# Performance work log

Hardware: AMD Instinct MI355X
Metric: run time of the kernel (lower is better)

The kernel has to match this reference:

```python
import jax, jax.numpy as jnp
import numpy as np

EMBED = 1024
NUM_HEADS = 8
HEAD_DIM = EMBED // NUM_HEADS // 2  # 64
LAMBDA_INIT = 0.8
EPS = 1e-5


def setup_inputs() -> dict:
    key = jax.random.key(0)
    ks = jax.random.split(key, 12)
    B, T = 2, 2048
    mk = lambda k, shape, s=1.0: (jax.random.normal(k, shape, dtype=jnp.float32) * s)
    return {
        "q": mk(ks[0], (B, T, EMBED)),
        "k": mk(ks[1], (B, T, EMBED)),
        "v": mk(ks[2], (B, T, EMBED)),
        "Wq": mk(ks[3], (EMBED, EMBED), EMBED ** -0.5),
        "Wk": mk(ks[4], (EMBED, EMBED), EMBED ** -0.5),
        "Wv": mk(ks[5], (EMBED, EMBED), EMBED ** -0.5),
        "Wo": mk(ks[6], (EMBED, EMBED), EMBED ** -0.5),
        "lambda_q1": mk(ks[7], (HEAD_DIM,), 0.1),
        "lambda_k1": mk(ks[8], (HEAD_DIM,), 0.1),
        "lambda_q2": mk(ks[9], (HEAD_DIM,), 0.1),
        "lambda_k2": mk(ks[10], (HEAD_DIM,), 0.1),
    }


def reference(q, k, v, Wq, Wk, Wv, Wo, lambda_q1, lambda_k1, lambda_q2, lambda_k2):
    B, T, E = q.shape
    H, d = NUM_HEADS, HEAD_DIM
    scaling = d ** -0.5
    # projections (torch Linear: x @ W^T)
    qh = (q @ Wq.T).reshape(B, T, 2 * H, d).transpose(0, 2, 1, 3) * scaling  # [B,2H,T,d]
    kh = (k @ Wk.T).reshape(B, T, 2 * H, d).transpose(0, 2, 1, 3)            # [B,2H,T,d]
    vh = (v @ Wv.T).reshape(B, T, H, 2 * d).transpose(0, 2, 1, 3)            # [B,H,T,2d]
    # dual softmax attention over doubled heads
    attn_weights = jnp.einsum("bhtd,bhsd->bhts", qh, kh)  # [B,2H,T,S]
    attn_weights = jax.nn.softmax(attn_weights, axis=-1)
    # lambda-weighted difference
    lambda_1 = jnp.exp(jnp.sum(lambda_q1 * lambda_k1))
    lambda_2 = jnp.exp(jnp.sum(lambda_q2 * lambda_k2))
    lambda_full = lambda_1 - lambda_2 + LAMBDA_INIT
    aw = attn_weights.reshape(B, H, 2, T, T)
    aw = aw[:, :, 0] - lambda_full * aw[:, :, 1]  # [B,H,T,S]
    attn = jnp.einsum("bhts,bhsd->bhtd", aw, vh)  # [B,H,T,2d]
    # RMSNorm over last dim (no affine), then rescale
    attn = attn * jax.lax.rsqrt(jnp.mean(attn * attn, axis=-1, keepdims=True) + EPS)
    attn = attn * (1.0 - LAMBDA_INIT)
    attn = attn.transpose(0, 2, 1, 3).reshape(B, T, H * 2 * d)
    return attn @ Wo.T
```

## Files before the change

kernel.cpp:

```cpp
#include <hip/hip_runtime.h>
#include <hip/hip_bf16.h>

typedef __bf16 bf16;
typedef __attribute__((ext_vector_type(8))) __bf16 bf16x8;
typedef __attribute__((ext_vector_type(4))) __bf16 bf16x4;
typedef __attribute__((ext_vector_type(4))) float f32x4;
typedef __attribute__((ext_vector_type(16))) float f32x16;

#define EMBED 1024
#define BB 2
#define TT 2048
#define NH 8
#define MROWS (BB * TT)

__device__ __forceinline__ void async_cp16(const void* g, void* s) {
    __builtin_amdgcn_global_load_lds((const __attribute__((address_space(1))) void*)g,
                                     (__attribute__((address_space(3))) void*)s, 16, 0, 0);
}

struct Cvt7 { const float* s[7]; bf16* d[7]; int n[7]; };

__global__ __launch_bounds__(256) void cvt_kernel(Cvt7 a) {
    const int sl = blockIdx.y;
    const float* __restrict__ s = a.s[sl];
    bf16* __restrict__ d = a.d[sl];
    int i = (blockIdx.x * 256 + threadIdx.x) * 8;
    if (i >= a.n[sl]) return;
    f32x4 x = *(const f32x4*)(s + i);
    f32x4 y = *(const f32x4*)(s + i + 4);
    bf16x8 o;
    o[0] = (bf16)x[0]; o[1] = (bf16)x[1]; o[2] = (bf16)x[2]; o[3] = (bf16)x[3];
    o[4] = (bf16)y[0]; o[5] = (bf16)y[1]; o[6] = (bf16)y[2]; o[7] = (bf16)y[3];
    *(bf16x8*)(d + i) = o;
}

struct ProjArgs { const bf16* A[3]; const bf16* Bw[3]; bf16* C[3]; float scale[3]; };

__global__ __launch_bounds__(256) void gemm_proj(ProjArgs g) {
    const int z = blockIdx.z;
    const bf16* __restrict__ A  = g.A[z];
    const bf16* __restrict__ Bw = g.Bw[z];
    bf16* __restrict__ C = g.C[z];
    const float scale = g.scale[z];
    const int bm = (z == 2) ? blockIdx.y : blockIdx.x;
    const int bn = (z == 2) ? blockIdx.x : blockIdx.y;
    const int ldc = (z == 2) ? 4096 : 1024;

    __shared__ __align__(16) bf16 sA[128 * 32];
    __shared__ __align__(16) bf16 sB[128 * 32];
    const int tid = threadIdx.x;
    const int wave = tid >> 6, lane = tid & 63;
    const int wRow = (wave >> 1) * 64, wCol = (wave & 1) * 64;
    const int fr = lane & 15, fq = lane >> 4;

    f32x4 acc[4][4] = {};

    const int r = tid >> 2, jd = tid & 3;
    const int js = jd ^ ((r >> 1) & 3);
    const bf16* Ab = A + (size_t)(bm * 128 + r) * 1024 + js * 8;
    const bf16* Bb = Bw + (size_t)(bn * 128 + r) * 1024 + js * 8;

    for (int k0 = 0; k0 < 1024; k0 += 32) {
        async_cp16(Ab + k0, &sA[r * 32 + jd * 8]);
        async_cp16(Ab + (size_t)64 * 1024 + k0, &sA[(r + 64) * 32 + jd * 8]);
        async_cp16(Bb + k0, &sB[r * 32 + jd * 8]);
        async_cp16(Bb + (size_t)64 * 1024 + k0, &sB[(r + 64) * 32 + jd * 8]);
        __syncthreads();
        const int sw = (fr >> 1) & 3;
        bf16x8 af[4], bfr[4];
#pragma unroll
        for (int i = 0; i < 4; i++) {
            af[i]  = *(const bf16x8*)&sA[(wRow + 16 * i + fr) * 32 + ((fq ^ sw) * 8)];
            bfr[i] = *(const bf16x8*)&sB[(wCol + 16 * i + fr) * 32 + ((fq ^ sw) * 8)];
        }
#pragma unroll
        for (int mi = 0; mi < 4; mi++)
#pragma unroll
            for (int ni = 0; ni < 4; ni++)
                acc[mi][ni] = __builtin_amdgcn_mfma_f32_16x16x32_bf16(af[mi], bfr[ni], acc[mi][ni], 0, 0, 0);
        __syncthreads();
    }

#pragma unroll
    for (int mi = 0; mi < 4; mi++)
#pragma unroll
        for (int ni = 0; ni < 4; ni++)
#pragma unroll
            for (int rr = 0; rr < 4; rr++) {
                int row = bm * 128 + wRow + 16 * mi + fq * 4 + rr;
                int col = bn * 128 + wCol + 16 * ni + fr;
                C[(size_t)row * ldc + col] = (bf16)(acc[mi][ni][rr] * scale);
            }
}

__global__ __launch_bounds__(256) void gemm_o(const bf16* __restrict__ A,
                                              const bf16* __restrict__ Bw,
                                              float* __restrict__ C) {
    __shared__ __align__(16) bf16 sA[128 * 32];
    __shared__ __align__(16) bf16 sB[64 * 32];
    const int tid = threadIdx.x;
    const int wave = tid >> 6, lane = tid & 63;
    const int wRow = (wave >> 1) * 64, wCol = (wave & 1) * 32;
    const int bm = blockIdx.x, bn = blockIdx.y;
    const int fr = lane & 15, fq = lane >> 4;

    f32x4 acc[4][2] = {};

    const int r = tid >> 2, jd = tid & 3;
    const int js = jd ^ ((r >> 1) & 3);
    const bf16* Ab = A + (size_t)(bm * 128 + r) * 1024 + js * 8;
    const bf16* Bb = Bw + (size_t)(bn * 64 + r) * 1024 + js * 8;

    for (int k0 = 0; k0 < 1024; k0 += 32) {
        async_cp16(Ab + k0, &sA[r * 32 + jd * 8]);
        async_cp16(Ab + (size_t)64 * 1024 + k0, &sA[(r + 64) * 32 + jd * 8]);
        async_cp16(Bb + k0, &sB[r * 32 + jd * 8]);
        __syncthreads();
        const int sw = (fr >> 1) & 3;
        bf16x8 af[4], bfr[2];
#pragma unroll
        for (int i = 0; i < 4; i++)
            af[i] = *(const bf16x8*)&sA[(wRow + 16 * i + fr) * 32 + ((fq ^ sw) * 8)];
#pragma unroll
        for (int i = 0; i < 2; i++)
            bfr[i] = *(const bf16x8*)&sB[(wCol + 16 * i + fr) * 32 + ((fq ^ sw) * 8)];
#pragma unroll
        for (int mi = 0; mi < 4; mi++)
#pragma unroll
            for (int ni = 0; ni < 2; ni++)
                acc[mi][ni] = __builtin_amdgcn_mfma_f32_16x16x32_bf16(af[mi], bfr[ni], acc[mi][ni], 0, 0, 0);
        __syncthreads();
    }

#pragma unroll
    for (int mi = 0; mi < 4; mi++)
#pragma unroll
        for (int ni = 0; ni < 2; ni++)
#pragma unroll
            for (int rr = 0; rr < 4; rr++) {
                int row = bm * 128 + wRow + 16 * mi + fq * 4 + rr;
                int col = bn * 64 + wCol + 16 * ni + fr;
                C[(size_t)row * 1024 + col] = acc[mi][ni][rr];
            }
}

__global__ __launch_bounds__(512, 2) void diff_attn_mfma(const bf16* __restrict__ Qp,
                                                         const bf16* __restrict__ Kp,
                                                         const bf16* __restrict__ Vt,
                                                         const float* __restrict__ lq1,
                                                         const float* __restrict__ lk1,
                                                         const float* __restrict__ lq2,
                                                         const float* __restrict__ lk2,
                                                         bf16* __restrict__ Out) {
    __shared__ __align__(16) char smem[65536];
    bf16* sK = (bf16*)smem;
    bf16* sV = (bf16*)(smem + 32768);

    const int tid = threadIdx.x;
    const int lane = tid & 63;
    const int wave = tid >> 6;
    const int l5 = lane & 31, q2 = lane >> 5;
    const int hd = wave & 1, qh = (wave >> 1) & 1, ks = wave >> 2;
    const int bh = blockIdx.y, b = bh >> 3, h = bh & 7;
    const int qt = blockIdx.x;

    float lam;
    {
        float a = lq1[lane] * lk1[lane];
        float c = lq2[lane] * lk2[lane];
#pragma unroll
        for (int off = 1; off < 64; off <<= 1) { a += __shfl_xor(a, off); c += __shfl_xor(c, off); }
        lam = __expf(a) - __expf(c) + 0.8f;
    }

    bf16x8 qf[2][4];
#pragma unroll
    for (int qrt = 0; qrt < 2; qrt++)
#pragma unroll
        for (int c = 0; c < 4; c++)
            qf[qrt][c] = *(const bf16x8*)(Qp + (size_t)(b * TT + qt * 128 + qh * 64 + qrt * 32 + l5) * 1024
                                          + h * 128 + hd * 64 + c * 16 + q2 * 8);

    f32x16 o[4][2] = {};
    float lp[2] = {0.f, 0.f};

    const bf16* Kbase = Kp + (size_t)(b * TT) * 1024 + h * 128;
    const bf16* Vbase = Vt + (size_t)(h * 128) * 4096 + b * TT;

#define STAGE_K(KT, BUF)                                                                   \
    {                                                                                      \
        bf16* dst = sK + (BUF) * 8192;                                                     \
        _Pragma("unroll") for (int i = 0; i < 2; i++) {                                    \
            int flat = i * 512 + tid;                                                      \
            int key = flat >> 4, ud = flat & 15, us = ud ^ (key & 15);                     \
            async_cp16(Kbase + (size_t)((KT) * 64 + key) * 1024 + us * 8, dst + flat * 8); \
        }                                                                                  \
    }
#define STAGE_V(KT, BUF)                                                                 \
    {                                                                                    \
        bf16* dst = sV + (BUF) * 8192;                                                   \
        _Pragma("unroll") for (int i = 0; i < 2; i++) {                                  \
            int flat = i * 512 + tid;                                                    \
            int dim = flat >> 3, ud = flat & 7, us = ud ^ (dim & 7);                     \
            async_cp16(Vbase + (size_t)dim * 4096 + (KT) * 64 + us * 8, dst + flat * 8); \
        }                                                                                \
    }

    STAGE_K(0, 0)
    STAGE_V(0, 0)
    __syncthreads();

    for (int kt = 0; kt < TT / 64; kt++) {
        if (kt + 1 < TT / 64) {
            STAGE_K(kt + 1, (kt + 1) & 1)
            STAGE_V(kt + 1, (kt + 1) & 1)
        }
        const bf16* cK = sK + (kt & 1) * 8192;
        const bf16* cV = sV + (kt & 1) * 8192;

        f32x16 s[2] = {};
        {
            const int key = ks * 32 + l5;
#pragma unroll
            for (int c = 0; c < 4; c++) {
                int u = (hd * 8 + c * 2 + q2) ^ (key & 15);
                bf16x8 kf = *(const bf16x8*)&cK[key * 128 + u * 8];
                s[0] = __builtin_amdgcn_mfma_f32_32x32x16_bf16(kf, qf[0][c], s[0], 0, 0, 0);
                s[1] = __builtin_amdgcn_mfma_f32_32x32x16_bf16(kf, qf[1][c], s[1], 0, 0, 0);
            }
        }

        bf16x8 pf[2][2];
#pragma unroll
        for (int qrt = 0; qrt < 2; qrt++) {
#pragma unroll
            for (int r = 0; r < 16; r++) {
                float p = __expf(s[qrt][r]);
                s[qrt][r] = p;
                lp[qrt] += p;
            }
#pragma unroll
            for (int c2 = 0; c2 < 2; c2++) {
                int pkk[2][2], xkk[2][2];
#pragma unroll
                for (int gg = 0; gg < 2; gg++) {
                    int g = 2 * c2 + gg;
                    bf16x4 t;
#pragma unroll
                    for (int rr = 0; rr < 4; rr++) t[rr] = (bf16)s[qrt][g * 4 + rr];
                    int2 u = *(int2*)&t;
                    pkk[gg][0] = u.x; pkk[gg][1] = u.y;
                    xkk[gg][0] = __shfl_xor(pkk[gg][0], 32);
                    xkk[gg][1] = __shfl_xor(pkk[gg][1], 32);
                }
                int4 ev;
                ev.x = q2 ? xkk[1][0] : pkk[0][0];
                ev.y = q2 ? xkk[1][1] : pkk[0][1];
                ev.z = q2 ? pkk[1][0] : xkk[0][0];
                ev.w = q2 ? pkk[1][1] : xkk[0][1];
                pf[qrt][c2] = *(bf16x8*)&ev;
            }
        }

#pragma unroll
        for (int dt = 0; dt < 4; dt++) {
            const int dim = dt * 32 + l5;
#pragma unroll
            for (int c2 = 0; c2 < 2; c2++) {
                int u = (ks * 4 + c2 * 2 + q2) ^ (dim & 7);
                bf16x8 vf = *(const bf16x8*)&cV[dim * 64 + u * 8];
                o[dt][0] = __builtin_amdgcn_mfma_f32_32x32x16_bf16(vf, pf[0][c2], o[dt][0], 0, 0, 0);
                o[dt][1] = __builtin_amdgcn_mfma_f32_32x32x16_bf16(vf, pf[1][c2], o[dt][1], 0, 0, 0);
            }
        }
        __syncthreads();
    }

    float* sL = (float*)(smem + 54272);
    {
        float ls0 = lp[0] + __shfl_xor(lp[0], 32);
        float ls1 = lp[1] + __shfl_xor(lp[1], 32);
        if (ks == 0 && q2 == 0) {
            sL[hd * 128 + qh * 64 + l5] = ls0;
            sL[hd * 128 + qh * 64 + 32 + l5] = ls1;
        }
        __syncthreads();
        if (ks == 1 && q2 == 0) {
            sL[hd * 128 + qh * 64 + l5] += ls0;
            sL[hd * 128 + qh * 64 + 32 + l5] += ls1;
        }
        __syncthreads();
    }

    float* sX = (float*)smem;
    for (int dt = 0; dt < 4; dt++) {
        if (ks == 1) {
#pragma unroll
            for (int qrt = 0; qrt < 2; qrt++) {
                float* t = sX + ((hd * 2 + qh) * 2 + qrt) * 1056;
#pragma unroll
                for (int r = 0; r < 16; r++) {
                    int row = (r & 3) + 8 * (r >> 2) + 4 * q2;
                    t[row * 33 + l5] = o[dt][qrt][r];
                }
            }
        }
        __syncthreads();
        if (ks == 0) {
#pragma unroll
            for (int qrt = 0; qrt < 2; qrt++) {
                const float* t = sX + ((hd * 2 + qh) * 2 + qrt) * 1056;
#pragma unroll
                for (int r = 0; r < 16; r++) {
                    int row = (r & 3) + 8 * (r >> 2) + 4 * q2;
                    o[dt][qrt][r] += t[row * 33 + l5];
                }
            }
        }
        __syncthreads();
    }

    float inv0[2], inv1[2];
    if (ks == 0 && hd == 0) {
#pragma unroll
        for (int qrt = 0; qrt < 2; qrt++) {
            int qr = qh * 64 + qrt * 32 + l5;
            inv0[qrt] = 1.0f / sL[qr];
            inv1[qrt] = lam / sL[128 + qr];
        }
    }

    float* sY = (float*)(smem + 36864);
    float ssacc[2] = {0.f, 0.f};
    for (int dt = 0; dt < 4; dt++) {
        if (ks == 0 && hd == 1) {
#pragma unroll
            for (int qrt = 0; qrt < 2; qrt++) {
                float* t = sY + (qh * 2 + qrt) * 1056;
#pragma unroll
                for (int r = 0; r < 16; r++) {
                    int row = (r & 3) + 8 * (r >> 2) + 4 * q2;
                    t[row * 33 + l5] = o[dt][qrt][r];
                }
            }
        }
        __syncthreads();
        if (ks == 0 && hd == 0) {
#pragma unroll
            for (int qrt = 0; qrt < 2; qrt++) {
                const float* t = sY + (qh * 2 + qrt) * 1056;
#pragma unroll
                for (int r = 0; r < 16; r++) {
                    int row = (r & 3) + 8 * (r >> 2) + 4 * q2;
                    float x = o[dt][qrt][r] * inv0[qrt] - inv1[qrt] * t[row * 33 + l5];
                    o[dt][qrt][r] = x;
                    ssacc[qrt] += x * x;
                }
            }
        }
        __syncthreads();
    }

    if (ks == 0 && hd == 0) {
#pragma unroll
        for (int qrt = 0; qrt < 2; qrt++) {
            float ss = ssacc[qrt] + __shfl_xor(ssacc[qrt], 32);
            float rs = rsqrtf(ss * (1.0f / 128.0f) + 1e-5f) * 0.2f;
            int row = b * TT + qt * 128 + qh * 64 + qrt * 32 + l5;
            bf16* op = Out + (size_t)row * 1024 + h * 128;
#pragma unroll
            for (int dt = 0; dt < 4; dt++)
#pragma unroll
                for (int rg = 0; rg < 4; rg++) {
                    bf16x4 w;
#pragma unroll
                    for (int rr = 0; rr < 4; rr++) w[rr] = (bf16)(o[dt][qrt][rg * 4 + rr] * rs);
                    int d0 = dt * 32 + rg * 8 + q2 * 4;
                    *(bf16x4*)&op[d0] = w;
                }
        }
    }
}

extern "C" void kernel_launch(void* const* d_in, const int* in_sizes, int n_in,
                              void* d_out, int out_size, void* d_ws, size_t ws_size,
                              hipStream_t stream) {
    const float* q   = (const float*)d_in[0];
    const float* k   = (const float*)d_in[1];
    const float* v   = (const float*)d_in[2];
    const float* Wq  = (const float*)d_in[3];
    const float* Wk  = (const float*)d_in[4];
    const float* Wv  = (const float*)d_in[5];
    const float* Wo  = (const float*)d_in[6];
    const float* lq1 = (const float*)d_in[7];
    const float* lk1 = (const float*)d_in[8];
    const float* lq2 = (const float*)d_in[9];
    const float* lk2 = (const float*)d_in[10];

    const size_t NACT = (size_t)MROWS * EMBED;
    const size_t NW   = (size_t)EMBED * EMBED;

    char* ws = (char*)d_ws;
    bf16* qb  = (bf16*)ws; ws += NACT * 2;
    bf16* kb  = (bf16*)ws; ws += NACT * 2;
    bf16* vb  = (bf16*)ws; ws += NACT * 2;
    bf16* Wqb = (bf16*)ws; ws += NW * 2;
    bf16* Wkb = (bf16*)ws; ws += NW * 2;
    bf16* Wvb = (bf16*)ws; ws += NW * 2;
    bf16* Wob = (bf16*)ws; ws += NW * 2;
    bf16* Qp  = (bf16*)ws; ws += NACT * 2;
    bf16* Kp  = (bf16*)ws; ws += NACT * 2;
    bf16* Vtp = (bf16*)ws; ws += NACT * 2;
    bf16* Ao  = (bf16*)ws; ws += NACT * 2;

    Cvt7 cv;
    cv.s[0] = q;  cv.s[1] = k;  cv.s[2] = v;
    cv.s[3] = Wq; cv.s[4] = Wk; cv.s[5] = Wv; cv.s[6] = Wo;
    cv.d[0] = qb;  cv.d[1] = kb;  cv.d[2] = vb;
    cv.d[3] = Wqb; cv.d[4] = Wkb; cv.d[5] = Wvb; cv.d[6] = Wob;
    cv.n[0] = cv.n[1] = cv.n[2] = (int)NACT;
    cv.n[3] = cv.n[4] = cv.n[5] = cv.n[6] = (int)NW;
    cvt_kernel<<<dim3((unsigned)(NACT / 2048), 7), 256, 0, stream>>>(cv);

    ProjArgs pa;
    pa.A[0] = qb;  pa.A[1] = kb;  pa.A[2] = Wvb;
    pa.Bw[0] = Wqb; pa.Bw[1] = Wkb; pa.Bw[2] = vb;
    pa.C[0] = Qp;  pa.C[1] = Kp;  pa.C[2] = Vtp;
    pa.scale[0] = 0.125f; pa.scale[1] = 1.0f; pa.scale[2] = 1.0f;
    gemm_proj<<<dim3(MROWS / 128, EMBED / 128, 3), 256, 0, stream>>>(pa);

    diff_attn_mfma<<<dim3(TT / 128, BB * NH), 512, 0, stream>>>(Qp, Kp, Vtp, lq1, lk1, lq2, lk2, Ao);

    gemm_o<<<dim3(MROWS / 128, EMBED / 64), 256, 0, stream>>>(Ao, Wob, (float*)d_out);

    (void)in_sizes; (void)n_in; (void)out_size; (void)ws_size;
}
```

Before: 234.2 us.

## Double-buffer projection GEMMs and shrink attention blocks to 64 query rows

Both projection GEMMs and the output GEMM get two LDS buffers, so the next k-slice is prefetched while MFMAs run on the current one. The attention kernel drops from 512 to 256 threads and from 128 to 64 query rows per block, doubling the grid to 512 blocks to improve occupancy and load balance. In exchange K/V tiles are reloaded twice as often per query, and the doubled LDS in the GEMMs may lower their occupancy. The single sync per iteration relies on the end-of-loop barrier to keep buffer reuse safe.

```diff
diff --git a/kernel.cpp b/kernel.cpp
--- a/kernel.cpp
+++ b/kernel.cpp
@@ -36,7 +36,7 @@
 
 struct ProjArgs { const bf16* A[3]; const bf16* Bw[3]; bf16* C[3]; float scale[3]; };
 
-__global__ __launch_bounds__(256) void gemm_proj(ProjArgs g) {
+__global__ __launch_bounds__(256, 3) void gemm_proj(ProjArgs g) {
     const int z = blockIdx.z;
     const bf16* __restrict__ A  = g.A[z];
     const bf16* __restrict__ Bw = g.Bw[z];
@@ -46,8 +46,8 @@
     const int bn = (z == 2) ? blockIdx.x : blockIdx.y;
     const int ldc = (z == 2) ? 4096 : 1024;
 
-    __shared__ __align__(16) bf16 sA[128 * 32];
-    __shared__ __align__(16) bf16 sB[128 * 32];
+    __shared__ __align__(16) bf16 sA[2][128 * 32];
+    __shared__ __align__(16) bf16 sB[2][128 * 32];
     const int tid = threadIdx.x;
     const int wave = tid >> 6, lane = tid & 63;
     const int wRow = (wave >> 1) * 64, wCol = (wave & 1) * 64;
@@ -60,18 +60,25 @@
     const bf16* Ab = A + (size_t)(bm * 128 + r) * 1024 + js * 8;
     const bf16* Bb = Bw + (size_t)(bn * 128 + r) * 1024 + js * 8;
 
-    for (int k0 = 0; k0 < 1024; k0 += 32) {
-        async_cp16(Ab + k0, &sA[r * 32 + jd * 8]);
-        async_cp16(Ab + (size_t)64 * 1024 + k0, &sA[(r + 64) * 32 + jd * 8]);
-        async_cp16(Bb + k0, &sB[r * 32 + jd * 8]);
-        async_cp16(Bb + (size_t)64 * 1024 + k0, &sB[(r + 64) * 32 + jd * 8]);
-        __syncthreads();
+#define PSTAGE(K0, BUF)                                              \
+    async_cp16(Ab + (K0), &sA[BUF][r * 32 + jd * 8]);                \
+    async_cp16(Ab + 65536 + (K0), &sA[BUF][(r + 64) * 32 + jd * 8]); \
+    async_cp16(Bb + (K0), &sB[BUF][r * 32 + jd * 8]);                \
+    async_cp16(Bb + 65536 + (K0), &sB[BUF][(r + 64) * 32 + jd * 8]);
+
+    PSTAGE(0, 0)
+    __syncthreads();
+
+    for (int it = 0; it < 32; it++) {
+        if (it + 1 < 32) { PSTAGE((it + 1) * 32, (it + 1) & 1) }
+        const bf16* cA = sA[it & 1];
+        const bf16* cB = sB[it & 1];
         const int sw = (fr >> 1) & 3;
         bf16x8 af[4], bfr[4];
 #pragma unroll
         for (int i = 0; i < 4; i++) {
-            af[i]  = *(const bf16x8*)&sA[(wRow + 16 * i + fr) * 32 + ((fq ^ sw) * 8)];
-            bfr[i] = *(const bf16x8*)&sB[(wCol + 16 * i + fr) * 32 + ((fq ^ sw) * 8)];
+            af[i]  = *(const bf16x8*)&cA[(wRow + 16 * i + fr) * 32 + ((fq ^ sw) * 8)];
+            bfr[i] = *(const bf16x8*)&cB[(wCol + 16 * i + fr) * 32 + ((fq ^ sw) * 8)];
         }
 #pragma unroll
         for (int mi = 0; mi < 4; mi++)
@@ -80,6 +87,7 @@
                 acc[mi][ni] = __builtin_amdgcn_mfma_f32_16x16x32_bf16(af[mi], bfr[ni], acc[mi][ni], 0, 0, 0);
         __syncthreads();
     }
+#undef PSTAGE
 
 #pragma unroll
     for (int mi = 0; mi < 4; mi++)
@@ -93,11 +101,11 @@
             }
 }
 
-__global__ __launch_bounds__(256) void gemm_o(const bf16* __restrict__ A,
-                                              const bf16* __restrict__ Bw,
-                                              float* __restrict__ C) {
-    __shared__ __align__(16) bf16 sA[128 * 32];
-    __shared__ __align__(16) bf16 sB[64 * 32];
+__global__ __launch_bounds__(256, 2) void gemm_o(const bf16* __restrict__ A,
+                                                 const bf16* __restrict__ Bw,
+                                                 float* __restrict__ C) {
+    __shared__ __align__(16) bf16 sA[2][128 * 32];
+    __shared__ __align__(16) bf16 sB[2][64 * 32];
     const int tid = threadIdx.x;
     const int wave = tid >> 6, lane = tid & 63;
     const int wRow = (wave >> 1) * 64, wCol = (wave & 1) * 32;
@@ -111,19 +119,26 @@
     const bf16* Ab = A + (size_t)(bm * 128 + r) * 1024 + js * 8;
     const bf16* Bb = Bw + (size_t)(bn * 64 + r) * 1024 + js * 8;
 
-    for (int k0 = 0; k0 < 1024; k0 += 32) {
-        async_cp16(Ab + k0, &sA[r * 32 + jd * 8]);
-        async_cp16(Ab + (size_t)64 * 1024 + k0, &sA[(r + 64) * 32 + jd * 8]);
-        async_cp16(Bb + k0, &sB[r * 32 + jd * 8]);
-        __syncthreads();
+#define OSTAGE(K0, BUF)                                              \
+    async_cp16(Ab + (K0), &sA[BUF][r * 32 + jd * 8]);                \
+    async_cp16(Ab + 65536 + (K0), &sA[BUF][(r + 64) * 32 + jd * 8]); \
+    async_cp16(Bb + (K0), &sB[BUF][r * 32 + jd * 8]);
+
+    OSTAGE(0, 0)
+    __syncthreads();
+
+    for (int it = 0; it < 32; it++) {
+        if (it + 1 < 32) { OSTAGE((it + 1) * 32, (it + 1) & 1) }
+        const bf16* cA = sA[it & 1];
+        const bf16* cB = sB[it & 1];
         const int sw = (fr >> 1) & 3;
         bf16x8 af[4], bfr[2];
 #pragma unroll
         for (int i = 0; i < 4; i++)
-            af[i] = *(const bf16x8*)&sA[(wRow + 16 * i + fr) * 32 + ((fq ^ sw) * 8)];
+            af[i] = *(const bf16x8*)&cA[(wRow + 16 * i + fr) * 32 + ((fq ^ sw) * 8)];
 #pragma unroll
         for (int i = 0; i < 2; i++)
-            bfr[i] = *(const bf16x8*)&sB[(wCol + 16 * i + fr) * 32 + ((fq ^ sw) * 8)];
+            bfr[i] = *(const bf16x8*)&cB[(wCol + 16 * i + fr) * 32 + ((fq ^ sw) * 8)];
 #pragma unroll
         for (int mi = 0; mi < 4; mi++)
 #pragma unroll
@@ -131,6 +146,7 @@
                 acc[mi][ni] = __builtin_amdgcn_mfma_f32_16x16x32_bf16(af[mi], bfr[ni], acc[mi][ni], 0, 0, 0);
         __syncthreads();
     }
+#undef OSTAGE
 
 #pragma unroll
     for (int mi = 0; mi < 4; mi++)
@@ -144,7 +160,7 @@
             }
 }
 
-__global__ __launch_bounds__(512, 2) void diff_attn_mfma(const bf16* __restrict__ Qp,
+__global__ __launch_bounds__(256, 4) void diff_attn_mfma(const bf16* __restrict__ Qp,
                                                          const bf16* __restrict__ Kp,
                                                          const bf16* __restrict__ Vt,
                                                          const float* __restrict__ lq1,
@@ -160,7 +176,7 @@
     const int lane = tid & 63;
     const int wave = tid >> 6;
     const int l5 = lane & 31, q2 = lane >> 5;
-    const int hd = wave & 1, qh = (wave >> 1) & 1, ks = wave >> 2;
+    const int hd = wave & 1, ks = wave >> 1;
     const int bh = blockIdx.y, b = bh >> 3, h = bh & 7;
     const int qt = blockIdx.x;
 
@@ -178,7 +194,7 @@
     for (int qrt = 0; qrt < 2; qrt++)
 #pragma unroll
         for (int c = 0; c < 4; c++)
-            qf[qrt][c] = *(const bf16x8*)(Qp + (size_t)(b * TT + qt * 128 + qh * 64 + qrt * 32 + l5) * 1024
+            qf[qrt][c] = *(const bf16x8*)(Qp + (size_t)(b * TT + qt * 64 + qrt * 32 + l5) * 1024
                                           + h * 128 + hd * 64 + c * 16 + q2 * 8);
 
     f32x16 o[4][2] = {};
@@ -190,8 +206,8 @@
 #define STAGE_K(KT, BUF)                                                                   \
     {                                                                                      \
         bf16* dst = sK + (BUF) * 8192;                                                     \
-        _Pragma("unroll") for (int i = 0; i < 2; i++) {                                    \
-            int flat = i * 512 + tid;                                                      \
+        _Pragma("unroll") for (int i = 0; i < 4; i++) {                                    \
+            int flat = i * 256 + tid;                                                      \
             int key = flat >> 4, ud = flat & 15, us = ud ^ (key & 15);                     \
             async_cp16(Kbase + (size_t)((KT) * 64 + key) * 1024 + us * 8, dst + flat * 8); \
         }                                                                                  \
@@ -199,8 +215,8 @@
 #define STAGE_V(KT, BUF)                                                                 \
     {                                                                                    \
         bf16* dst = sV + (BUF) * 8192;                                                   \
-        _Pragma("unroll") for (int i = 0; i < 2; i++) {                                  \
-            int flat = i * 512 + tid;                                                    \
+        _Pragma("unroll") for (int i = 0; i < 4; i++) {                                  \
+            int flat = i * 256 + tid;                                                    \
             int dim = flat >> 3, ud = flat & 7, us = ud ^ (dim & 7);                     \
             async_cp16(Vbase + (size_t)dim * 4096 + (KT) * 64 + us * 8, dst + flat * 8); \
         }                                                                                \
@@ -281,13 +297,13 @@
         float ls0 = lp[0] + __shfl_xor(lp[0], 32);
         float ls1 = lp[1] + __shfl_xor(lp[1], 32);
         if (ks == 0 && q2 == 0) {
-            sL[hd * 128 + qh * 64 + l5] = ls0;
-            sL[hd * 128 + qh * 64 + 32 + l5] = ls1;
+            sL[hd * 64 + l5] = ls0;
+            sL[hd * 64 + 32 + l5] = ls1;
         }
         __syncthreads();
         if (ks == 1 && q2 == 0) {
-            sL[hd * 128 + qh * 64 + l5] += ls0;
-            sL[hd * 128 + qh * 64 + 32 + l5] += ls1;
+            sL[hd * 64 + l5] += ls0;
+            sL[hd * 64 + 32 + l5] += ls1;
         }
         __syncthreads();
     }
@@ -297,7 +313,7 @@
         if (ks == 1) {
 #pragma unroll
             for (int qrt = 0; qrt < 2; qrt++) {
-                float* t = sX + ((hd * 2 + qh) * 2 + qrt) * 1056;
+                float* t = sX + (hd * 2 + qrt) * 1056;
 #pragma unroll
                 for (int r = 0; r < 16; r++) {
                     int row = (r & 3) + 8 * (r >> 2) + 4 * q2;
@@ -309,7 +325,7 @@
         if (ks == 0) {
 #pragma unroll
             for (int qrt = 0; qrt < 2; qrt++) {
-                const float* t = sX + ((hd * 2 + qh) * 2 + qrt) * 1056;
+                const float* t = sX + (hd * 2 + qrt) * 1056;
 #pragma unroll
                 for (int r = 0; r < 16; r++) {
                     int row = (r & 3) + 8 * (r >> 2) + 4 * q2;
@@ -324,9 +340,9 @@
     if (ks == 0 && hd == 0) {
 #pragma unroll
         for (int qrt = 0; qrt < 2; qrt++) {
-            int qr = qh * 64 + qrt * 32 + l5;
+            int qr = qrt * 32 + l5;
             inv0[qrt] = 1.0f / sL[qr];
-            inv1[qrt] = lam / sL[128 + qr];
+            inv1[qrt] = lam / sL[64 + qr];
         }
     }
 
@@ -336,7 +352,7 @@
         if (ks == 0 && hd == 1) {
 #pragma unroll
             for (int qrt = 0; qrt < 2; qrt++) {
-                float* t = sY + (qh * 2 + qrt) * 1056;
+                float* t = sY + qrt * 1056;
 #pragma unroll
                 for (int r = 0; r < 16; r++) {
                     int row = (r & 3) + 8 * (r >> 2) + 4 * q2;
@@ -348,7 +364,7 @@
         if (ks == 0 && hd == 0) {
 #pragma unroll
             for (int qrt = 0; qrt < 2; qrt++) {
-                const float* t = sY + (qh * 2 + qrt) * 1056;
+                const float* t = sY + qrt * 1056;
 #pragma unroll
                 for (int r = 0; r < 16; r++) {
                     int row = (r & 3) + 8 * (r >> 2) + 4 * q2;
@@ -366,7 +382,7 @@
         for (int qrt = 0; qrt < 2; qrt++) {
             float ss = ssacc[qrt] + __shfl_xor(ssacc[qrt], 32);
             float rs = rsqrtf(ss * (1.0f / 128.0f) + 1e-5f) * 0.2f;
-            int row = b * TT + qt * 128 + qh * 64 + qrt * 32 + l5;
+            int row = b * TT + qt * 64 + qrt * 32 + l5;
             bf16* op = Out + (size_t)row * 1024 + h * 128;
 #pragma unroll
             for (int dt = 0; dt < 4; dt++)
@@ -429,7 +445,7 @@
     pa.scale[0] = 0.125f; pa.scale[1] = 1.0f; pa.scale[2] = 1.0f;
     gemm_proj<<<dim3(MROWS / 128, EMBED / 128, 3), 256, 0, stream>>>(pa);
 
-    diff_attn_mfma<<<dim3(TT / 128, BB * NH), 512, 0, stream>>>(Qp, Kp, Vtp, lq1, lk1, lq2, lk2, Ao);
+    diff_attn_mfma<<<dim3(TT / 64, BB * NH), 256, 0, stream>>>(Qp, Kp, Vtp, lq1, lk1, lq2, lk2, Ao);
 
     gemm_o<<<dim3(MROWS / 128, EMBED / 64), 256, 0, stream>>>(Ao, Wob, (float*)d_out);
 
```

New measurement: 274.3 us. 1.17x slower.
